# Kernel optimization log

Hardware: AMD Instinct MI355X
Metric: run time of the kernel (lower is better)

Reference implementation:

```python
import jax, jax.numpy as jnp
import numpy as np
import math

BIT = 8
N_HEAD = 12

def quantize_k(x, k=BIT):
    # DoReFa k-bit uniform quantizer with straight-through estimator
    n = float(2 ** k - 1)
    q = jnp.round(x * n) / n
    return x + jax.lax.stop_gradient(q - x)

def weight_quant(w, k=BIT):
    # DoReFa weight quantization: tanh normalize to [0,1], quantize, map back to [-1,1]
    t = jnp.tanh(w)
    t = t / (2.0 * jnp.max(jnp.abs(t))) + 0.5
    return 2.0 * quantize_k(t, k) - 1.0

def act_quant(x, k=BIT):
    # DoReFa activation quantization: clamp to [0,1] then k-bit quantize
    return quantize_k(jnp.clip(x, 0.0, 1.0), k)

def setup_inputs() -> dict:
    key = jax.random.key(0)
    k1, k2, k3 = jax.random.split(key, 3)
    B, S, NX = 8, 1024, 768
    x = jax.random.normal(k1, (B, S, NX), dtype=jnp.float32)
    W_attn = 0.02 * jax.random.normal(k2, (NX, 3 * NX), dtype=jnp.float32)
    b_attn = jnp.zeros((3 * NX,), dtype=jnp.float32)
    W_proj = 0.02 * jax.random.normal(k3, (NX, NX), dtype=jnp.float32)
    b_proj = jnp.zeros((NX,), dtype=jnp.float32)
    return {"x": x, "W_attn": W_attn, "b_attn": b_attn, "W_proj": W_proj, "b_proj": b_proj}

def reference(x, W_attn, b_attn, W_proj, b_proj):
    B, S, NX = x.shape
    H = N_HEAD
    hd = NX // H
    # quantized c_attn (Conv1D)
    qkv = jnp.einsum('bsn,nf->bsf', x, weight_quant(W_attn)) + b_attn  # [B,S,3*NX]
    q, k, v = jnp.split(qkv, 3, axis=-1)
    def split_heads(t):
        return t.reshape(B, S, H, hd).transpose(0, 2, 1, 3)  # [B,H,S,hd]
    q = act_quant(split_heads(q))
    k = act_quant(split_heads(k))
    v = act_quant(split_heads(v))
    # manual causal attention, scale=True
    w = jnp.einsum('bhqd,bhkd->bhqk', q, k) / math.sqrt(hd)  # [B,H,S,S]
    mask = jnp.tril(jnp.ones((S, S), dtype=x.dtype))
    w = w * mask - 10000.0 * (1.0 - mask)
    w = jax.nn.softmax(w, axis=-1)
    a = jnp.einsum('bhqk,bhkd->bhqd', w, v)  # [B,H,S,hd]
    a = a.transpose(0, 2, 1, 3).reshape(B, S, NX)  # merge heads
    a = jnp.einsum('bsn,nf->bsf', a, weight_quant(W_proj)) + b_proj
    # present = stack(key.transpose(-2,-1), value) -> both [B,H,S,hd]
    present = jnp.stack((k, v))
    return (a, present)
```

## Files before the change

kernel.cpp:

```cpp
#include <hip/hip_runtime.h>
#include <math.h>

#define B_   8
#define S_   1024
#define NXc  768
#define H_   12
#define HDc  64
#define M_   (B_*S_)
#define NQKV (3*NXc)

typedef __attribute__((ext_vector_type(8))) short short8;
typedef __attribute__((ext_vector_type(8))) _Float16 half8;
typedef __attribute__((ext_vector_type(4))) float f32x4;

__device__ inline unsigned short f2h(float f) {
  union { _Float16 h; unsigned short u; } c;
  c.h = (_Float16)f;
  return c.u;
}

__device__ inline void gl_lds16(const unsigned short* g, unsigned short* l) {
  __builtin_amdgcn_global_load_lds(
      (const __attribute__((address_space(1))) void*)g,
      (__attribute__((address_space(3))) void*)l, 16, 0, 0);
}

static const size_t UA_OFF_F  = 0;
static const size_t UA_F_CNT  = ((size_t)NQKV * NXc + 1) / 2;
static const size_t UP_OFF_F  = UA_OFF_F + UA_F_CNT;
static const size_t UP_F_CNT  = ((size_t)NXc * NXc + 1) / 2;
static const size_t QH_OFF_F  = UP_OFF_F + UP_F_CNT;
static const size_t HALF_CNT  = ((size_t)M_ * NXc + 1) / 2;
static const size_t KH_OFF_F  = QH_OFF_F + HALF_CNT;
static const size_t VHT_OFF_F = KH_OFF_F + HALF_CNT;
static const size_t AHF_OFF_F = VHT_OFF_F + HALF_CNT;
static const size_t SC_OFF    = AHF_OFF_F + HALF_CNT;
static const size_t WS_FLOATS_NEEDED = SC_OFF + 2;

__global__ void k_maxtanh2(const float* __restrict__ wa, const float* __restrict__ wp,
                           unsigned int* __restrict__ out) {
  const int which = blockIdx.y;
  const float* w = which ? wp : wa;
  const int n = which ? (NXc * NXc) : (NXc * NQKV);
  float mx = 0.f;
  for (int i = blockIdx.x * blockDim.x + threadIdx.x; i < n;
       i += gridDim.x * blockDim.x)
    mx = fmaxf(mx, fabsf(tanhf(w[i])));
#pragma unroll
  for (int off = 32; off > 0; off >>= 1)
    mx = fmaxf(mx, __shfl_xor(mx, off));
  if ((threadIdx.x & 63) == 0)
    atomicMax(out + which, __float_as_uint(mx));
}

__global__ __launch_bounds__(256) void k_quantw_t(
    const float* __restrict__ w, unsigned short* __restrict__ ut,
    int K, int N, const unsigned int* __restrict__ gmax_bits) {
  __shared__ unsigned short Ut[64][72];
  const float inv2m = 0.5f / __uint_as_float(*gmax_bits);
  const int k0 = blockIdx.y * 64, n0 = blockIdx.x * 64;
  const int t = threadIdx.x;
  const int r = t >> 4, c4 = (t & 15) * 4;
#pragma unroll
  for (int rr = 0; rr < 4; ++rr) {
    int row = rr * 16 + r;
    float4 f = *(const float4*)(w + (size_t)(k0 + row) * N + n0 + c4);
    float fv[4] = {f.x, f.y, f.z, f.w};
#pragma unroll
    for (int j = 0; j < 4; ++j) {
      float tq = tanhf(fv[j]) * inv2m + 0.5f;
      float u = 2.0f * rintf(tq * 255.0f) - 255.0f;
      Ut[c4 + j][row] = f2h(u);
    }
  }
  __syncthreads();
#pragma unroll
  for (int rep = 0; rep < 2; ++rep) {
    int c = t + rep * 256;
    int n = c >> 3, slot = c & 7;
    short8 v = *(const short8*)&Ut[n][slot * 8];
    *(short8*)(ut + (size_t)(n0 + n) * K + k0 + slot * 8) = v;
  }
}

__global__ __launch_bounds__(256) void k_xhalf(
    const float* __restrict__ x, unsigned short* __restrict__ xh, int n8) {
  int i = blockIdx.x * 256 + threadIdx.x;
  if (i >= n8) return;
  const float* src = x + (size_t)i * 8;
  float4 f0 = *(const float4*)src;
  float4 f1 = *(const float4*)(src + 4);
  float fv[8] = {f0.x, f0.y, f0.z, f0.w, f1.x, f1.y, f1.z, f1.w};
  union { short8 v; unsigned short u[8]; } o;
#pragma unroll
  for (int j = 0; j < 8; ++j) o.u[j] = f2h(fv[j]);
  *(short8*)(xh + (size_t)i * 8) = o.v;
}

template <int EPI>
__global__ __launch_bounds__(256, 3) void k_gemm3(
    const unsigned short* __restrict__ Ag, const unsigned short* __restrict__ Ug,
    const float* __restrict__ bias, float* __restrict__ Cout,
    unsigned short* __restrict__ qh, unsigned short* __restrict__ kh,
    unsigned short* __restrict__ vht, float* __restrict__ kq, float* __restrict__ vq,
    int nbn) {
  __shared__ __align__(16) unsigned short SMEM[3 * 4096 * 2];
  unsigned short* Ahb3 = SMEM;
  unsigned short* Bsb3 = SMEM + 3 * 4096;
  unsigned short* T    = SMEM;

  const int bid = blockIdx.x;
  const int cpx = gridDim.x >> 3;
  const int swz = (bid & 7) * cpx + (bid >> 3);
  const int bm = swz / nbn, bn = swz % nbn;
  const int part = (EPI == 1) ? (bn / 6) : 0;

  const int t = threadIdx.x;
  const int w = t >> 6, lane = t & 63;
  const int wm = w >> 1, wn = w & 1;
  const int g = lane >> 4, ln = lane & 15;

  const unsigned short* Ab = Ag + (size_t)bm * 128 * NXc;
  const unsigned short* Bb = Ug + (size_t)bn * 128 * NXc;

  const int srow = t >> 2;
  const int aco  = (((t & 3) ^ ((t >> 3) & 3)) << 3);
  const int rsw  = ((g ^ ((ln >> 1) & 3)) << 3);

  f32x4 acc[4][4];
#pragma unroll
  for (int i = 0; i < 4; ++i)
#pragma unroll
    for (int j = 0; j < 4; ++j) acc[i][j] = (f32x4)(0.f);

  auto STAGE = [&](int tk, int buf) {
    const int k0 = tk * 32;
    unsigned short* Ah = Ahb3 + buf * 4096;
    unsigned short* Bs = Bsb3 + buf * 4096;
    gl_lds16(Ab + (size_t)srow * NXc + k0 + aco, &Ah[t * 8]);
    gl_lds16(Ab + (size_t)(srow + 64) * NXc + k0 + aco, &Ah[(256 + t) * 8]);
    gl_lds16(Bb + (size_t)srow * NXc + k0 + aco, &Bs[t * 8]);
    gl_lds16(Bb + (size_t)(srow + 64) * NXc + k0 + aco, &Bs[(256 + t) * 8]);
  };
  auto COMPUTE = [&](int buf) {
    const unsigned short* Ah = Ahb3 + buf * 4096;
    const unsigned short* Bs = Bsb3 + buf * 4096;
    half8 bfrag[4];
#pragma unroll
    for (int nf = 0; nf < 4; ++nf)
      bfrag[nf] = *(const half8*)&Bs[(wn * 64 + nf * 16 + ln) * 32 + rsw];
#pragma unroll
    for (int mf = 0; mf < 4; ++mf) {
      half8 ah = *(const half8*)&Ah[(wm * 64 + mf * 16 + ln) * 32 + rsw];
#pragma unroll
      for (int nf = 0; nf < 4; ++nf)
        acc[mf][nf] = __builtin_amdgcn_mfma_f32_16x16x32_f16(ah, bfrag[nf], acc[mf][nf], 0, 0, 0);
    }
  };

  STAGE(0, 0);
  STAGE(1, 1);
  for (int tk = 0; tk < 22; ++tk) {
    asm volatile("s_waitcnt vmcnt(4)" ::: "memory");
    __builtin_amdgcn_s_barrier();
    __builtin_amdgcn_sched_barrier(0);
    STAGE(tk + 2, (tk + 2) % 3);
    COMPUTE(tk % 3);
  }
  asm volatile("s_waitcnt vmcnt(4)" ::: "memory");
  __builtin_amdgcn_s_barrier();
  __builtin_amdgcn_sched_barrier(0);
  COMPUTE(22 % 3);
  asm volatile("s_waitcnt vmcnt(0)" ::: "memory");
  __builtin_amdgcn_s_barrier();
  __builtin_amdgcn_sched_barrier(0);
  COMPUTE(23 % 3);

  const float inv255 = 1.0f / 255.0f;
  if (EPI == 0) {
#pragma unroll
    for (int mf = 0; mf < 4; ++mf) {
      int row0 = bm * 128 + wm * 64 + mf * 16 + g * 4;
#pragma unroll
      for (int nf = 0; nf < 4; ++nf) {
        int col = bn * 128 + wn * 64 + nf * 16 + ln;
        float bv = bias[col];
#pragma unroll
        for (int r = 0; r < 4; ++r)
          Cout[(size_t)(row0 + r) * NXc + col] = acc[mf][nf][r] * inv255 + bv;
      }
    }
  } else if (part == 2) {
    __syncthreads();
#pragma unroll
    for (int mf = 0; mf < 4; ++mf) {
      int row0 = bm * 128 + wm * 64 + mf * 16 + g * 4;
#pragma unroll
      for (int nf = 0; nf < 4; ++nf) {
        int col = bn * 128 + wn * 64 + nf * 16 + ln;
        float bv255 = bias[col] * 255.0f;
        int ff = col - 2 * NXc;
        int h = ff >> 6, d = ff & 63;
        int c = wn * 64 + nf * 16 + ln;
#pragma unroll
        for (int r = 0; r < 4; ++r) {
          float y255 = rintf(fminf(fmaxf(acc[mf][nf][r] + bv255, 0.f), 255.f));
          int row = row0 + r;
          int b = row >> 10, s = row & 1023;
          vq[(((size_t)b * H_ + h) * S_ + s) * HDc + d] = y255 * inv255;
          int sl = wm * 64 + mf * 16 + g * 4 + r;
          T[c * 136 + sl] = f2h(y255);
        }
      }
    }
    __syncthreads();
    const int bB = bm >> 3;
    const int s0 = (bm & 7) * 128;
    const int h0 = (bn - 12) * 2;
#pragma unroll
    for (int rep = 0; rep < 8; ++rep) {
      int idx = rep * 256 + t;
      int c = idx >> 4, sc = idx & 15;
      short8 v = *(const short8*)&T[c * 136 + sc * 8];
      int h = h0 + (c >> 6), d = c & 63;
      *(short8*)(vht + (((size_t)bB * H_ + h) * HDc + d) * S_ + s0 + sc * 8) = v;
    }
  } else {
    __syncthreads();
#pragma unroll
    for (int mf = 0; mf < 4; ++mf) {
      int lrow0 = wm * 64 + mf * 16 + g * 4;
#pragma unroll
      for (int nf = 0; nf < 4; ++nf) {
        int lcol = wn * 64 + nf * 16 + ln;
        float bv255 = bias[bn * 128 + lcol] * 255.0f;
#pragma unroll
        for (int r = 0; r < 4; ++r) {
          float y255 = rintf(fminf(fmaxf(acc[mf][nf][r] + bv255, 0.f), 255.f));
          T[(lrow0 + r) * 136 + lcol] = f2h(y255);
        }
      }
    }
    __syncthreads();
#pragma unroll
    for (int rep = 0; rep < 8; ++rep) {
      int idx = rep * 256 + t;
      int row = idx >> 4, cc = idx & 15;
      short8 v = *(const short8*)&T[row * 136 + cc * 8];
      int grow = bm * 128 + row;
      int b = grow >> 10, s = grow & 1023;
      int col = bn * 128 + cc * 8;
      int ff = col - part * NXc;
      int h = ff >> 6, d0 = ff & 63;
      size_t dst = (((size_t)b * H_ + h) * S_ + s) * HDc + d0;
      if (part == 0) {
        *(short8*)(qh + dst) = v;
      } else {
        *(short8*)(kh + dst) = v;
        union { short8 s8; half8 h8; } cvt; cvt.s8 = v;
        float4 f0, f1;
        f0.x = (float)cvt.h8[0] * inv255; f0.y = (float)cvt.h8[1] * inv255;
        f0.z = (float)cvt.h8[2] * inv255; f0.w = (float)cvt.h8[3] * inv255;
        f1.x = (float)cvt.h8[4] * inv255; f1.y = (float)cvt.h8[5] * inv255;
        f1.z = (float)cvt.h8[6] * inv255; f1.w = (float)cvt.h8[7] * inv255;
        *(float4*)(kq + dst) = f0;
        *(float4*)(kq + dst + 4) = f1;
      }
    }
  }
}

__global__ __launch_bounds__(256) void k_attn_pair(
    const unsigned short* __restrict__ qh, const unsigned short* __restrict__ kh,
    const unsigned short* __restrict__ vht, unsigned short* __restrict__ ahf) {
  __shared__ __align__(16) unsigned short Ks[2][64 * 64];
  __shared__ __align__(16) unsigned short Vt[2][64 * 64];
  __shared__ __align__(16) unsigned short Pp[4 * 16 * 64];

  const int bid = blockIdx.x;
  const int gidx = (bid & 7) * 96 + (bid >> 3);
  const int hid = gidx >> 3;
  const int p = gidx & 7;
  const int b = hid / H_, h = hid - b * H_;

  const size_t hoff = (size_t)hid * S_ * HDc;
  const unsigned short* qhp = qh + hoff;
  const unsigned short* khp = kh + hoff;
  const unsigned short* vhp = vht + hoff;

  const int t = threadIdx.x;
  const int w = t >> 6, lane = t & 63;
  const int g = lane >> 4, ln = lane & 15;

  const int r0 = t >> 3, c0 = (((t & 7) ^ (r0 & 7)) << 3);
  const int r1 = 32 + (t >> 3), c1 = (((t & 7) ^ (r1 & 7)) << 3);

  auto STAGE = [&](int jb, int buf) {
    gl_lds16(khp + (size_t)(jb * 64 + r0) * HDc + c0, &Ks[buf][t * 8]);
    gl_lds16(khp + (size_t)(jb * 64 + r1) * HDc + c1, &Ks[buf][(256 + t) * 8]);
    gl_lds16(vhp + (size_t)r0 * S_ + jb * 64 + c0, &Vt[buf][t * 8]);
    gl_lds16(vhp + (size_t)r1 * S_ + jb * 64 + c1, &Vt[buf][(256 + t) * 8]);
  };

  const float SCALE = 1.0f / (255.0f * 255.0f * 8.0f);

  int iq = p;
  half8 qfrag[2];
  {
    const unsigned short* qr = qhp + (size_t)(iq * 64 + w * 16 + ln) * HDc;
    qfrag[0] = *(const half8*)(qr + g * 8);
    qfrag[1] = *(const half8*)(qr + 32 + g * 8);
  }

  float l[4];
  f32x4 accO[4];
#pragma unroll
  for (int r = 0; r < 4; ++r) l[r] = 0.f;
#pragma unroll
  for (int nf = 0; nf < 4; ++nf) accO[nf] = (f32x4)(0.f);

  auto WRITEOUT = [&]() {
#pragma unroll
    for (int off = 1; off < 16; off <<= 1)
#pragma unroll
      for (int r = 0; r < 4; ++r) l[r] += __shfl_xor(l[r], off);
#pragma unroll
    for (int r = 0; r < 4; ++r) {
      float inv = 1.0f / (255.0f * l[r]);
      size_t row = (size_t)b * S_ + iq * 64 + w * 16 + g * 4 + r;
#pragma unroll
      for (int nf = 0; nf < 4; ++nf)
        ahf[row * NXc + h * HDc + nf * 16 + ln] = f2h(accO[nf][r] * inv);
    }
  };

  STAGE(0, 0);
  int jb = 0;
  for (int i = 0; i < 17; ++i) {
    const int buf = i & 1;
    __syncthreads();
    if (i + 1 < 17) {
      int njb = (i + 1 <= p) ? (i + 1) : (i - p);
      STAGE(njb, buf ^ 1);
    }

    f32x4 accS[4];
#pragma unroll
    for (int nf = 0; nf < 4; ++nf) accS[nf] = (f32x4)(0.f);
#pragma unroll
    for (int ks = 0; ks < 2; ++ks)
#pragma unroll
      for (int nf = 0; nf < 4; ++nf) {
        int kvr = nf * 16 + ln;
        half8 bk = *(const half8*)&Ks[buf][kvr * 64 + ((ks * 32 + g * 8) ^ ((kvr & 7) << 3))];
        accS[nf] = __builtin_amdgcn_mfma_f32_16x16x32_f16(qfrag[ks], bk, accS[nf], 0, 0, 0);
      }

    float pr[4][4];
    if (jb == iq) {
      const int grow = iq * 64 + w * 16 + g * 4;
      const int gcol = jb * 64 + ln;
#pragma unroll
      for (int nf = 0; nf < 4; ++nf)
#pragma unroll
        for (int r = 0; r < 4; ++r) {
          float pv = (gcol + nf * 16 > grow + r) ? 0.f : __expf(accS[nf][r] * SCALE);
          pr[nf][r] = pv;
          l[r] += pv;
        }
    } else {
#pragma unroll
      for (int nf = 0; nf < 4; ++nf)
#pragma unroll
        for (int r = 0; r < 4; ++r) {
          float pv = __expf(accS[nf][r] * SCALE);
          pr[nf][r] = pv;
          l[r] += pv;
        }
    }

#pragma unroll
    for (int nf = 0; nf < 4; ++nf)
#pragma unroll
      for (int r = 0; r < 4; ++r) {
        int prow = g * 4 + r;
        Pp[w * 1024 + prow * 64 + ((nf * 16 + ln) ^ ((prow & 7) << 3))] = f2h(pr[nf][r]);
      }

#pragma unroll
    for (int ks = 0; ks < 2; ++ks) {
      half8 pa = *(const half8*)&Pp[w * 1024 + ln * 64 + ((ks * 32 + g * 8) ^ ((ln & 7) << 3))];
#pragma unroll
      for (int nf = 0; nf < 4; ++nf) {
        int d = nf * 16 + ln;
        half8 bv = *(const half8*)&Vt[buf][d * 64 + ((ks * 32 + g * 8) ^ ((d & 7) << 3))];
        accO[nf] = __builtin_amdgcn_mfma_f32_16x16x32_f16(pa, bv, accO[nf], 0, 0, 0);
      }
    }

    if (i == p) {
      WRITEOUT();
#pragma unroll
      for (int r = 0; r < 4; ++r) l[r] = 0.f;
#pragma unroll
      for (int nf = 0; nf < 4; ++nf) accO[nf] = (f32x4)(0.f);
      iq = 15 - p;
      const unsigned short* qr2 = qhp + (size_t)(iq * 64 + w * 16 + ln) * HDc;
      qfrag[0] = *(const half8*)(qr2 + g * 8);
      qfrag[1] = *(const half8*)(qr2 + 32 + g * 8);
    } else if (i == 16) {
      WRITEOUT();
    }
    jb = (i + 1 <= p) ? (i + 1) : (i - p);
  }
}

extern "C" void kernel_launch(void* const* d_in, const int* in_sizes, int n_in,
                              void* d_out, int out_size, void* d_ws, size_t ws_size,
                              hipStream_t stream) {
  const float* x      = (const float*)d_in[0];
  const float* W_attn = (const float*)d_in[1];
  const float* b_attn = (const float*)d_in[2];
  const float* W_proj = (const float*)d_in[3];
  const float* b_proj = (const float*)d_in[4];

  float* out = (float*)d_out;
  float* ws  = (float*)d_ws;
  if (ws_size < WS_FLOATS_NEEDED * sizeof(float)) return;

  float* a_out = out;
  float* k_out = out + (size_t)M_ * NXc;
  float* v_out = k_out + (size_t)M_ * NXc;

  unsigned short* ua  = (unsigned short*)(ws + UA_OFF_F);
  unsigned short* up  = (unsigned short*)(ws + UP_OFF_F);
  unsigned short* qh  = (unsigned short*)(ws + QH_OFF_F);
  unsigned short* kh  = (unsigned short*)(ws + KH_OFF_F);
  unsigned short* vht = (unsigned short*)(ws + VHT_OFF_F);
  unsigned short* ahf = (unsigned short*)(ws + AHF_OFF_F);
  unsigned int* sc = (unsigned int*)(ws + SC_OFF);

  unsigned short* xh = ahf;

  hipMemsetAsync(sc, 0, 2 * sizeof(unsigned int), stream);

  k_maxtanh2<<<dim3(128, 2), 256, 0, stream>>>(W_attn, W_proj, sc);

  k_quantw_t<<<dim3(NQKV / 64, NXc / 64), 256, 0, stream>>>(W_attn, ua, NXc, NQKV, sc);
  k_quantw_t<<<dim3(NXc / 64, NXc / 64), 256, 0, stream>>>(W_proj, up, NXc, NXc, sc + 1);

  k_xhalf<<<(M_ * NXc / 8 + 255) / 256, 256, 0, stream>>>(x, xh, M_ * NXc / 8);

  k_gemm3<1><<<(NQKV / 128) * (M_ / 128), 256, 0, stream>>>(
      xh, ua, b_attn, nullptr, qh, kh, vht, k_out, v_out, NQKV / 128);

  k_attn_pair<<<768, 256, 0, stream>>>(qh, kh, vht, ahf);

  k_gemm3<0><<<(NXc / 128) * (M_ / 128), 256, 0, stream>>>(
      ahf, up, b_proj, a_out, nullptr, nullptr, nullptr, nullptr, nullptr, NXc / 128);
}
```

Measured before the change: 142.2 us.

## Split GEMM into QKV 128x256 tile kernel and proj 64x128 tile kernel

The templated GEMM is replaced by two specialized kernels. The QKV projection now uses 512-thread blocks computing 128x256 tiles, so each A tile is reused across twice as many columns and the grid shrinks to 576 blocks. The output projection uses 64x128 tiles, doubling its block count to 768 for better CU coverage on the smaller GEMM. Costs are higher LDS use and more registers per block in the QKV kernel, which may reduce occupancy. The epilogue indexing is also more complex, including a 264-stride staging buffer.

```diff
diff --git a/kernel.cpp b/kernel.cpp
--- a/kernel.cpp
+++ b/kernel.cpp
@@ -97,31 +97,28 @@
   *(short8*)(xh + (size_t)i * 8) = o.v;
 }
 
-template <int EPI>
-__global__ __launch_bounds__(256, 3) void k_gemm3(
-    const unsigned short* __restrict__ Ag, const unsigned short* __restrict__ Ug,
-    const float* __restrict__ bias, float* __restrict__ Cout,
+__global__ __launch_bounds__(512, 4) void k_gemm_qkv(
+    const unsigned short* __restrict__ xh, const unsigned short* __restrict__ ua,
+    const float* __restrict__ bias,
     unsigned short* __restrict__ qh, unsigned short* __restrict__ kh,
-    unsigned short* __restrict__ vht, float* __restrict__ kq, float* __restrict__ vq,
-    int nbn) {
-  __shared__ __align__(16) unsigned short SMEM[3 * 4096 * 2];
+    unsigned short* __restrict__ vht, float* __restrict__ kq, float* __restrict__ vq) {
+  __shared__ __align__(16) unsigned short SMEM[3 * (4096 + 8192)];
   unsigned short* Ahb3 = SMEM;
   unsigned short* Bsb3 = SMEM + 3 * 4096;
   unsigned short* T    = SMEM;
 
   const int bid = blockIdx.x;
-  const int cpx = gridDim.x >> 3;
-  const int swz = (bid & 7) * cpx + (bid >> 3);
-  const int bm = swz / nbn, bn = swz % nbn;
-  const int part = (EPI == 1) ? (bn / 6) : 0;
+  const int swz = (bid & 7) * 72 + (bid >> 3);
+  const int bm = swz / 9, bn = swz % 9;
+  const int part = bn / 3;
 
   const int t = threadIdx.x;
   const int w = t >> 6, lane = t & 63;
-  const int wm = w >> 1, wn = w & 1;
+  const int wm = w >> 2, wn = w & 3;
   const int g = lane >> 4, ln = lane & 15;
 
-  const unsigned short* Ab = Ag + (size_t)bm * 128 * NXc;
-  const unsigned short* Bb = Ug + (size_t)bn * 128 * NXc;
+  const unsigned short* Ab = xh + (size_t)bm * 128 * NXc;
+  const unsigned short* Bb = ua + (size_t)bn * 256 * NXc;
 
   const int srow = t >> 2;
   const int aco  = (((t & 3) ^ ((t >> 3) & 3)) << 3);
@@ -136,15 +133,14 @@
   auto STAGE = [&](int tk, int buf) {
     const int k0 = tk * 32;
     unsigned short* Ah = Ahb3 + buf * 4096;
-    unsigned short* Bs = Bsb3 + buf * 4096;
+    unsigned short* Bs = Bsb3 + buf * 8192;
     gl_lds16(Ab + (size_t)srow * NXc + k0 + aco, &Ah[t * 8]);
-    gl_lds16(Ab + (size_t)(srow + 64) * NXc + k0 + aco, &Ah[(256 + t) * 8]);
     gl_lds16(Bb + (size_t)srow * NXc + k0 + aco, &Bs[t * 8]);
-    gl_lds16(Bb + (size_t)(srow + 64) * NXc + k0 + aco, &Bs[(256 + t) * 8]);
+    gl_lds16(Bb + (size_t)(srow + 128) * NXc + k0 + aco, &Bs[(512 + t) * 8]);
   };
   auto COMPUTE = [&](int buf) {
     const unsigned short* Ah = Ahb3 + buf * 4096;
-    const unsigned short* Bs = Bsb3 + buf * 4096;
+    const unsigned short* Bs = Bsb3 + buf * 8192;
     half8 bfrag[4];
 #pragma unroll
     for (int nf = 0; nf < 4; ++nf)
@@ -161,13 +157,13 @@
   STAGE(0, 0);
   STAGE(1, 1);
   for (int tk = 0; tk < 22; ++tk) {
-    asm volatile("s_waitcnt vmcnt(4)" ::: "memory");
+    asm volatile("s_waitcnt vmcnt(3)" ::: "memory");
     __builtin_amdgcn_s_barrier();
     __builtin_amdgcn_sched_barrier(0);
     STAGE(tk + 2, (tk + 2) % 3);
     COMPUTE(tk % 3);
   }
-  asm volatile("s_waitcnt vmcnt(4)" ::: "memory");
+  asm volatile("s_waitcnt vmcnt(3)" ::: "memory");
   __builtin_amdgcn_s_barrier();
   __builtin_amdgcn_sched_barrier(0);
   COMPUTE(22 % 3);
@@ -177,31 +173,18 @@
   COMPUTE(23 % 3);
 
   const float inv255 = 1.0f / 255.0f;
-  if (EPI == 0) {
+  if (part == 2) {
+    __syncthreads();
 #pragma unroll
     for (int mf = 0; mf < 4; ++mf) {
       int row0 = bm * 128 + wm * 64 + mf * 16 + g * 4;
 #pragma unroll
       for (int nf = 0; nf < 4; ++nf) {
-        int col = bn * 128 + wn * 64 + nf * 16 + ln;
-        float bv = bias[col];
-#pragma unroll
-        for (int r = 0; r < 4; ++r)
-          Cout[(size_t)(row0 + r) * NXc + col] = acc[mf][nf][r] * inv255 + bv;
-      }
-    }
-  } else if (part == 2) {
-    __syncthreads();
-#pragma unroll
-    for (int mf = 0; mf < 4; ++mf) {
-      int row0 = bm * 128 + wm * 64 + mf * 16 + g * 4;
-#pragma unroll
-      for (int nf = 0; nf < 4; ++nf) {
-        int col = bn * 128 + wn * 64 + nf * 16 + ln;
+        int c = wn * 64 + nf * 16 + ln;
+        int col = bn * 256 + c;
         float bv255 = bias[col] * 255.0f;
         int ff = col - 2 * NXc;
         int h = ff >> 6, d = ff & 63;
-        int c = wn * 64 + nf * 16 + ln;
 #pragma unroll
         for (int r = 0; r < 4; ++r) {
           float y255 = rintf(fminf(fmaxf(acc[mf][nf][r] + bv255, 0.f), 255.f));
@@ -216,10 +199,10 @@
     __syncthreads();
     const int bB = bm >> 3;
     const int s0 = (bm & 7) * 128;
-    const int h0 = (bn - 12) * 2;
+    const int h0 = (bn - 6) * 4;
 #pragma unroll
     for (int rep = 0; rep < 8; ++rep) {
-      int idx = rep * 256 + t;
+      int idx = rep * 512 + t;
       int c = idx >> 4, sc = idx & 15;
       short8 v = *(const short8*)&T[c * 136 + sc * 8];
       int h = h0 + (c >> 6), d = c & 63;
@@ -233,23 +216,23 @@
 #pragma unroll
       for (int nf = 0; nf < 4; ++nf) {
         int lcol = wn * 64 + nf * 16 + ln;
-        float bv255 = bias[bn * 128 + lcol] * 255.0f;
+        float bv255 = bias[bn * 256 + lcol] * 255.0f;
 #pragma unroll
         for (int r = 0; r < 4; ++r) {
           float y255 = rintf(fminf(fmaxf(acc[mf][nf][r] + bv255, 0.f), 255.f));
-          T[(lrow0 + r) * 136 + lcol] = f2h(y255);
+          T[(lrow0 + r) * 264 + lcol] = f2h(y255);
         }
       }
     }
     __syncthreads();
 #pragma unroll
     for (int rep = 0; rep < 8; ++rep) {
-      int idx = rep * 256 + t;
-      int row = idx >> 4, cc = idx & 15;
-      short8 v = *(const short8*)&T[row * 136 + cc * 8];
+      int idx = rep * 512 + t;
+      int row = idx >> 5, cc = idx & 31;
+      short8 v = *(const short8*)&T[row * 264 + cc * 8];
       int grow = bm * 128 + row;
       int b = grow >> 10, s = grow & 1023;
-      int col = bn * 128 + cc * 8;
+      int col = bn * 256 + cc * 8;
       int ff = col - part * NXc;
       int h = ff >> 6, d0 = ff & 63;
       size_t dst = (((size_t)b * H_ + h) * S_ + s) * HDc + d0;
@@ -270,6 +253,92 @@
   }
 }
 
+__global__ __launch_bounds__(256, 4) void k_gemm_proj(
+    const unsigned short* __restrict__ ahf, const unsigned short* __restrict__ up,
+    const float* __restrict__ bias, float* __restrict__ Cout) {
+  __shared__ __align__(16) unsigned short SMEM[3 * (2048 + 4096)];
+  unsigned short* Ahb3 = SMEM;
+  unsigned short* Bsb3 = SMEM + 3 * 2048;
+
+  const int bid = blockIdx.x;
+  const int swz = (bid & 7) * 96 + (bid >> 3);
+  const int bm = swz / 6, bn = swz % 6;
+
+  const int t = threadIdx.x;
+  const int w = t >> 6, lane = t & 63;
+  const int wm = w >> 1, wn = w & 1;
+  const int g = lane >> 4, ln = lane & 15;
+
+  const unsigned short* Ab = ahf + (size_t)bm * 64 * NXc;
+  const unsigned short* Bb = up + (size_t)bn * 128 * NXc;
+
+  const int srow = t >> 2;
+  const int aco  = (((t & 3) ^ ((t >> 3) & 3)) << 3);
+  const int rsw  = ((g ^ ((ln >> 1) & 3)) << 3);
+
+  f32x4 acc[2][4];
+#pragma unroll
+  for (int i = 0; i < 2; ++i)
+#pragma unroll
+    for (int j = 0; j < 4; ++j) acc[i][j] = (f32x4)(0.f);
+
+  auto STAGE = [&](int tk, int buf) {
+    const int k0 = tk * 32;
+    unsigned short* Ah = Ahb3 + buf * 2048;
+    unsigned short* Bs = Bsb3 + buf * 4096;
+    gl_lds16(Ab + (size_t)srow * NXc + k0 + aco, &Ah[t * 8]);
+    gl_lds16(Bb + (size_t)srow * NXc + k0 + aco, &Bs[t * 8]);
+    gl_lds16(Bb + (size_t)(srow + 64) * NXc + k0 + aco, &Bs[(256 + t) * 8]);
+  };
+  auto COMPUTE = [&](int buf) {
+    const unsigned short* Ah = Ahb3 + buf * 2048;
+    const unsigned short* Bs = Bsb3 + buf * 4096;
+    half8 bfrag[4];
+#pragma unroll
+    for (int nf = 0; nf < 4; ++nf)
+      bfrag[nf] = *(const half8*)&Bs[(wn * 64 + nf * 16 + ln) * 32 + rsw];
+#pragma unroll
+    for (int mf = 0; mf < 2; ++mf) {
+      half8 ah = *(const half8*)&Ah[(wm * 32 + mf * 16 + ln) * 32 + rsw];
+#pragma unroll
+      for (int nf = 0; nf < 4; ++nf)
+        acc[mf][nf] = __builtin_amdgcn_mfma_f32_16x16x32_f16(ah, bfrag[nf], acc[mf][nf], 0, 0, 0);
+    }
+  };
+
+  STAGE(0, 0);
+  STAGE(1, 1);
+  for (int tk = 0; tk < 22; ++tk) {
+    asm volatile("s_waitcnt vmcnt(3)" ::: "memory");
+    __builtin_amdgcn_s_barrier();
+    __builtin_amdgcn_sched_barrier(0);
+    STAGE(tk + 2, (tk + 2) % 3);
+    COMPUTE(tk % 3);
+  }
+  asm volatile("s_waitcnt vmcnt(3)" ::: "memory");
+  __builtin_amdgcn_s_barrier();
+  __builtin_amdgcn_sched_barrier(0);
+  COMPUTE(22 % 3);
+  asm volatile("s_waitcnt vmcnt(0)" ::: "memory");
+  __builtin_amdgcn_s_barrier();
+  __builtin_amdgcn_sched_barrier(0);
+  COMPUTE(23 % 3);
+
+  const float inv255 = 1.0f / 255.0f;
+#pragma unroll
+  for (int mf = 0; mf < 2; ++mf) {
+    int row0 = bm * 64 + wm * 32 + mf * 16 + g * 4;
+#pragma unroll
+    for (int nf = 0; nf < 4; ++nf) {
+      int col = bn * 128 + wn * 64 + nf * 16 + ln;
+      float bv = bias[col];
+#pragma unroll
+      for (int r = 0; r < 4; ++r)
+        Cout[(size_t)(row0 + r) * NXc + col] = acc[mf][nf][r] * inv255 + bv;
+    }
+  }
+}
+
 __global__ __launch_bounds__(256) void k_attn_pair(
     const unsigned short* __restrict__ qh, const unsigned short* __restrict__ kh,
     const unsigned short* __restrict__ vht, unsigned short* __restrict__ ahf) {
@@ -451,11 +520,10 @@
 
   k_xhalf<<<(M_ * NXc / 8 + 255) / 256, 256, 0, stream>>>(x, xh, M_ * NXc / 8);
 
-  k_gemm3<1><<<(NQKV / 128) * (M_ / 128), 256, 0, stream>>>(
-      xh, ua, b_attn, nullptr, qh, kh, vht, k_out, v_out, NQKV / 128);
+  k_gemm_qkv<<<(NQKV / 256) * (M_ / 128), 512, 0, stream>>>(
+      xh, ua, b_attn, qh, kh, vht, k_out, v_out);
 
   k_attn_pair<<<768, 256, 0, stream>>>(qh, kh, vht, ahf);
 
-  k_gemm3<0><<<(NXc / 128) * (M_ / 128), 256, 0, stream>>>(
-      ahf, up, b_proj, a_out, nullptr, nullptr, nullptr, nullptr, nullptr, NXc / 128);
-}
+  k_gemm_proj<<<(NXc / 128) * (M_ / 64), 256, 0, stream>>>(ahf, up, b_proj, a_out);
+}
```

Measured after the change: 143.8 us. Within noise of the previous version (+1.1%).
